# Performance work log

Measured on AMD Instinct MI355X. Metric: run time of the kernel, lower is better.

## Reference

```python
import jax, jax.numpy as jnp
import numpy as np


def grid_sample_bilinear(img, grid):
    """Replicates torch F.grid_sample(mode='bilinear', padding_mode='zeros',
    align_corners=False). img: [B,C,Hin,Win]; grid: [B,Ho,Wo,2] in [-1,1]
    with grid[...,0]=x (width), grid[...,1]=y (height). Returns [B,C,Ho,Wo]."""
    B, C, Hin, Win = img.shape
    x = (grid[..., 0] + 1.0) * (Win * 0.5) - 0.5  # unnormalized pixel coords
    y = (grid[..., 1] + 1.0) * (Hin * 0.5) - 0.5
    x0 = jnp.floor(x)
    y0 = jnp.floor(y)
    wx1 = x - x0
    wy1 = y - y0

    def tap(xi, yi, w):
        valid = ((xi >= 0) & (xi < Win) & (yi >= 0) & (yi < Hin)).astype(img.dtype)
        xc = jnp.clip(xi, 0, Win - 1).astype(jnp.int32)
        yc = jnp.clip(yi, 0, Hin - 1).astype(jnp.int32)
        def gather_one(im, yb, xb, wb):
            return im[:, yb, xb] * wb[None]  # [C,Ho,Wo]
        return jax.vmap(gather_one)(img, yc, xc, valid * w)

    return (tap(x0, y0, (1.0 - wx1) * (1.0 - wy1))
            + tap(x0 + 1.0, y0, wx1 * (1.0 - wy1))
            + tap(x0, y0 + 1.0, (1.0 - wx1) * wy1)
            + tap(x0 + 1.0, y0 + 1.0, wx1 * wy1))


def setup_inputs() -> dict:
    key = jax.random.key(0)
    k_uv, k1, k2, k3, k4 = jax.random.split(key, 5)
    W, H = 2048, 2048
    B, Ho, Wo = 8, 1024, 1024
    return {
        "uv": jax.random.uniform(k_uv, (B, Ho, Wo, 2), dtype=jnp.float32),
        "layer1": jax.random.normal(k1, (1, 1, W, H), dtype=jnp.float32),
        "layer2": jax.random.normal(k2, (1, 1, W // 2, H // 2), dtype=jnp.float32),
        "layer3": jax.random.normal(k3, (1, 1, W // 4, H // 4), dtype=jnp.float32),
        "layer4": jax.random.normal(k4, (1, 1, W // 8, H // 8), dtype=jnp.float32),
    }


def reference(uv, layer1, layer2, layer3, layer4):
    B = uv.shape[0]
    grid = uv * 2.0 - 1.0
    y = None
    for layer in (layer1, layer2, layer3, layer4):
        img = jnp.broadcast_to(layer, (B,) + layer.shape[1:])  # repeat(B,1,1,1)
        s = grid_sample_bilinear(img, grid)
        y = s if y is None else y + s
    return y  # [B,1,Ho,Wo]
```

## Files before the change

kernel.cpp:

```cpp
#include <hip/hip_runtime.h>
#include <hip/hip_fp16.h>


typedef unsigned int u32x2 __attribute__((ext_vector_type(2)));
typedef unsigned int u32x4 __attribute__((ext_vector_type(4)));
typedef float f32x4 __attribute__((ext_vector_type(4)));

#define K 1024
#define CHUNK 4096
#define HB 4096
#define SEG (CHUNK * 256)
#define NXCD 8

__device__ __forceinline__ int binof(float u, float v) {
    int bx = min(max((int)(u * 32.0f), 0), 31);
    int by = min(max((int)(v * 32.0f), 0), 31);
    return by * 32 + bx;
}

__device__ __forceinline__ unsigned pack2(float lo, float hi) {
    __half2 h = __halves2half2(__float2half(lo), __float2half(hi));
    unsigned w;
    __builtin_memcpy(&w, &h, 4);
    return w;
}

__global__ __launch_bounds__(256) void repack_hist_kernel(
    const float* __restrict__ l1, const float* __restrict__ l2,
    const float* __restrict__ l3, const float* __restrict__ l4,
    __half2* __restrict__ r1, __half2* __restrict__ r2,
    __half2* __restrict__ r3, __half2* __restrict__ r4,
    const float2* __restrict__ uv, unsigned* __restrict__ seghist,
    unsigned* __restrict__ chist, int n) {
    const int n1 = 2048 * 2048, n2 = 1024 * 1024, n3 = 512 * 512, n4 = 256 * 256;
    {
        int e = (blockIdx.x * 256 + threadIdx.x) * 4;
        const float* __restrict__ src = nullptr;
        __half2* __restrict__ dst = nullptr;
        int S = 0, logS = 0, j = 0;
        if (e < n1) {
            src = l1; dst = r1; S = 2048; logS = 11; j = e;
        } else if (e < n1 + n2) {
            src = l2; dst = r2; S = 1024; logS = 10; j = e - n1;
        } else if (e < n1 + n2 + n3) {
            src = l3; dst = r3; S = 512; logS = 9; j = e - (n1 + n2);
        } else if (e < n1 + n2 + n3 + n4) {
            src = l4; dst = r4; S = 256; logS = 8; j = e - (n1 + n2 + n3);
        }
        if (src) {
            int y = j >> logS;
            f32x4 a = *(const f32x4*)(src + j);
            f32x4 b = *(const f32x4*)(src + ((y < S - 1) ? (j + S) : j));
            u32x4 o = {pack2(a.x, b.x), pack2(a.y, b.y), pack2(a.z, b.z),
                       pack2(a.w, b.w)};
            *(u32x4*)(dst + j) = o;
        }
    }
    if (seghist == nullptr) return;
    int c = blockIdx.x;
    int base = c * HB;
    if (base >= n) return;
    __shared__ unsigned cnt[K];
    for (int b = threadIdx.x; b < K; b += 256) cnt[b] = 0u;
    __syncthreads();
    int m = min(HB, n - base);
    const f32x4* uv4 = (const f32x4*)(uv + base);
    int npair = m >> 1;
    for (int k2 = threadIdx.x; k2 < npair; k2 += 256) {
        f32x4 q = __builtin_nontemporal_load(&uv4[k2]);
        atomicAdd(&cnt[binof(q.x, q.y)], 1u);
        atomicAdd(&cnt[binof(q.z, q.w)], 1u);
    }
    if ((m & 1) && threadIdx.x == 0) {
        float2 q = uv[base + m - 1];
        atomicAdd(&cnt[binof(q.x, q.y)], 1u);
    }
    __syncthreads();
    int seg = base / SEG;
    unsigned* gh = seghist + (size_t)seg * K;
    for (int b = threadIdx.x; b < K; b += 256) {
        unsigned v = cnt[b];
        if (chist) chist[(size_t)c * K + b] = v;
        if (v) atomicAdd(&gh[b], v);
    }
}

__global__ __launch_bounds__(256) void cursor_kernel(
    const unsigned* __restrict__ seghist, const unsigned* __restrict__ chist,
    unsigned* __restrict__ cursor, int nchunks) {
    int seg = blockIdx.x >> 6;
    int grp = blockIdx.x & 63;
    const unsigned* h = seghist + (size_t)seg * K;
    __shared__ unsigned part[256];
    __shared__ unsigned base[K];
    int t = threadIdx.x;
    unsigned v0 = h[t * 4], v1 = h[t * 4 + 1], v2 = h[t * 4 + 2], v3 = h[t * 4 + 3];
    unsigned s1 = v0, s2 = v0 + v1, s3 = v0 + v1 + v2;
    part[t] = s3 + v3;
    __syncthreads();
    for (int off = 1; off < 256; off <<= 1) {
        unsigned x = (t >= off) ? part[t - off] : 0u;
        __syncthreads();
        part[t] += x;
        __syncthreads();
    }
    unsigned tb = (t > 0) ? part[t - 1] : 0u;
    unsigned segstart = (unsigned)seg * (unsigned)SEG;
    base[t * 4] = segstart + tb;
    base[t * 4 + 1] = segstart + tb + s1;
    base[t * 4 + 2] = segstart + tb + s2;
    base[t * 4 + 3] = segstart + tb + s3;
    __syncthreads();
    int wave = t >> 6, lane = t & 63;
    int c0 = seg * (SEG / CHUNK);
    for (int j = wave; j < 16; j += 4) {
        int b = grp * 16 + j;
        unsigned run = 0;
        for (int r = 0; r < 4; ++r) {
            int c = r * 64 + lane;
            unsigned v = (c0 + c < nchunks) ? chist[(size_t)(c0 + c) * K + b] : 0u;
            unsigned x = v;
            for (int d = 1; d < 64; d <<= 1) {
                unsigned y = __shfl_up(x, d);
                if (lane >= d) x += y;
            }
            cursor[((size_t)seg * K + b) * 256 + c] = base[b] + (x - v) + run;
            run += __shfl(x, 63);
        }
    }
}

__global__ __launch_bounds__(256) void partition_kernel(
    const float2* __restrict__ uv, const unsigned* __restrict__ chist,
    const unsigned* __restrict__ cursor, float2* __restrict__ uv_s,
    unsigned* __restrict__ invp, int n, int pinned) {
    __shared__ float2 ssort[CHUNK];
    __shared__ unsigned cnt[K];
    __shared__ unsigned lbase[K];
    __shared__ unsigned gdiff[K];
    __shared__ unsigned part[256];
    int t = threadIdx.x;
    int blk = blockIdx.x;
    int c = pinned ? ((blk % NXCD) * (SEG / CHUNK) + blk / NXCD) : blk;
    int cb = c * CHUNK;
    if (cb >= n) return;
    int cnum = min(CHUNK, n - cb);
    int seg = c / (SEG / CHUNK);
    int cidx = c % (SEG / CHUNK);

    u32x4 hv = *(const u32x4*)(chist + (size_t)c * K + t * 4);
    {
        unsigned s1 = hv.x, s2 = hv.x + hv.y, s3 = hv.x + hv.y + hv.z;
        part[t] = s3 + hv.w;
        __syncthreads();
        for (int off = 1; off < 256; off <<= 1) {
            unsigned x = (t >= off) ? part[t - off] : 0u;
            __syncthreads();
            part[t] += x;
            __syncthreads();
        }
        unsigned tb = (t > 0) ? part[t - 1] : 0u;
        unsigned lb[4] = {tb, tb + s1, tb + s2, tb + s3};
        for (int j = 0; j < 4; ++j) {
            int b = t * 4 + j;
            lbase[b] = lb[j];
            gdiff[b] = cursor[((size_t)seg * K + b) * (SEG / CHUNK) + cidx] - lb[j];
            cnt[b] = 0u;
        }
    }
    __syncthreads();
    const f32x4* uv4 = (const f32x4*)(uv + cb);
    int npair = cnum >> 1;
    for (int k2 = t; k2 < npair; k2 += 256) {
        f32x4 q = uv4[k2];
        int ba = binof(q.x, q.y);
        unsigned sa = lbase[ba] + atomicAdd(&cnt[ba], 1u);
        ssort[sa] = make_float2(q.x, q.y);
        int bb = binof(q.z, q.w);
        unsigned sb = lbase[bb] + atomicAdd(&cnt[bb], 1u);
        ssort[sb] = make_float2(q.z, q.w);
        if (invp) {
            u32x2 iv;
            iv.x = gdiff[ba] + sa;
            iv.y = gdiff[bb] + sb;
            *(u32x2*)(invp + cb + k2 * 2) = iv;
        }
    }
    if ((cnum & 1) && t == 0) {
        float2 q = uv[cb + cnum - 1];
        int b = binof(q.x, q.y);
        unsigned s = lbase[b] + atomicAdd(&cnt[b], 1u);
        ssort[s] = q;
        if (invp) invp[cb + cnum - 1] = gdiff[b] + s;
    }
    __syncthreads();
    for (int s = t; s < cnum; s += 256) {
        float2 q = ssort[s];
        int b = binof(q.x, q.y);
        uv_s[gdiff[b] + (unsigned)s] = q;
    }
}

__global__ __launch_bounds__(256) void partition_idx_kernel(
    const float2* __restrict__ uv, const unsigned* __restrict__ hist,
    unsigned* __restrict__ cursor, float2* __restrict__ uv_s,
    unsigned* __restrict__ idxp, int n, int pinned) {
    __shared__ float2 suv[CHUNK];
    __shared__ unsigned short slid[CHUNK];
    __shared__ unsigned cnt[K];
    __shared__ unsigned lbase[K];
    __shared__ unsigned goff[K];
    __shared__ unsigned part[256];
    int t = threadIdx.x;
    int blk = blockIdx.x;
    int c = pinned ? ((blk % NXCD) * (SEG / CHUNK) + blk / NXCD) : blk;
    int cb = c * CHUNK;
    if (cb >= n) return;
    int cnum = min(CHUNK, n - cb);
    int seg = cb / SEG;
    unsigned segstart = (unsigned)((size_t)seg * SEG);
    {
        const f32x4* uv4 = (const f32x4*)(uv + cb);
        int npair = cnum >> 1;
        for (int k2 = t; k2 < npair; k2 += 256) {
            f32x4 q = uv4[k2];
            suv[k2 * 2] = make_float2(q.x, q.y);
            suv[k2 * 2 + 1] = make_float2(q.z, q.w);
        }
        if ((cnum & 1) && t == 0) suv[cnum - 1] = uv[cb + cnum - 1];
    }
    for (int b = t; b < K; b += 256) cnt[b] = 0u;
    __syncthreads();
    for (int k = t; k < cnum; k += 256)
        atomicAdd(&cnt[binof(suv[k].x, suv[k].y)], 1u);
    __syncthreads();
    {
        unsigned v0 = cnt[t * 4], v1 = cnt[t * 4 + 1], v2 = cnt[t * 4 + 2],
                 v3 = cnt[t * 4 + 3];
        unsigned s1 = v0, s2 = v0 + v1, s3 = v0 + v1 + v2;
        part[t] = s3 + v3;
        __syncthreads();
        for (int off = 1; off < 256; off <<= 1) {
            unsigned x = (t >= off) ? part[t - off] : 0u;
            __syncthreads();
            part[t] += x;
            __syncthreads();
        }
        unsigned tb = (t > 0) ? part[t - 1] : 0u;
        lbase[t * 4] = tb;
        lbase[t * 4 + 1] = tb + s1;
        lbase[t * 4 + 2] = tb + s2;
        lbase[t * 4 + 3] = tb + s3;
    }
    __syncthreads();
    {
        const unsigned* h = hist + (size_t)seg * K;
        unsigned v0 = h[t * 4], v1 = h[t * 4 + 1], v2 = h[t * 4 + 2],
                 v3 = h[t * 4 + 3];
        unsigned s1 = v0, s2 = v0 + v1, s3 = v0 + v1 + v2;
        part[t] = s3 + v3;
        __syncthreads();
        for (int off = 1; off < 256; off <<= 1) {
            unsigned x = (t >= off) ? part[t - off] : 0u;
            __syncthreads();
            part[t] += x;
            __syncthreads();
        }
        unsigned tb = (t > 0) ? part[t - 1] : 0u;
        unsigned sbv[4] = {tb, tb + s1, tb + s2, tb + s3};
        for (int j = 0; j < 4; ++j) {
            int b = t * 4 + j;
            unsigned cc = cnt[b];
            unsigned r = cc ? atomicAdd(&cursor[(size_t)seg * K + b], cc) : 0u;
            goff[b] = segstart + sbv[j] + r;
        }
    }
    __syncthreads();
    for (int b = t; b < K; b += 256) cnt[b] = 0u;
    __syncthreads();
    for (int k = t; k < cnum; k += 256) {
        int b = binof(suv[k].x, suv[k].y);
        unsigned r = atomicAdd(&cnt[b], 1u);
        slid[lbase[b] + r] = (unsigned short)k;
    }
    __syncthreads();
    for (int s = t; s < cnum; s += 256) {
        int lid = slid[s];
        float2 q = suv[lid];
        int b = binof(q.x, q.y);
        unsigned pos = goff[b] + ((unsigned)s - lbase[b]);
        uv_s[pos] = q;
        idxp[pos] = (unsigned)(cb + lid);
    }
}

__device__ __forceinline__ float sample_level(const __half2* __restrict__ R,
                                              const int S, const float gx,
                                              const float gy) {
    const float halfS = 0.5f * (float)S;
    float x = (gx + 1.0f) * halfS - 0.5f;
    float y = (gy + 1.0f) * halfS - 0.5f;
    float xf = floorf(x), yf = floorf(y);
    float wx = x - xf, wy = y - yf;
    int x0 = (int)xf, y0 = (int)yf;

    int yc = min(max(y0, 0), S - 1);
    float wa = (y0 >= 0) ? (1.0f - wy) : wy;
    if (y0 < -1 || y0 >= S) wa = 0.0f;
    float wb = (y0 >= 0 && y0 < S - 1) ? wy : 0.0f;

    int xb = min(max(x0, 0), S - 2);
    bool xin = (x0 >= 0) && (x0 <= S - 2);
    float wxa = xin ? (1.0f - wx) : ((x0 == -1) ? wx : 0.0f);
    float wxb = xin ? wx : ((x0 == S - 1) ? (1.0f - wx) : 0.0f);

    uint2 q;
    __builtin_memcpy(&q, (const char*)(R + (size_t)yc * (size_t)S + xb), 8);
    __half2 ca = *(const __half2*)&q.x;
    __half2 cb = *(const __half2*)&q.y;
    float2 fa = __half22float2(ca);
    float2 fb = __half22float2(cb);
    float cola = fmaf(wa, fa.x, wb * fa.y);
    float colb = fmaf(wa, fb.x, wb * fb.y);
    return fmaf(wxa, cola, wxb * colb);
}

__device__ __forceinline__ float sample_point(const __half2* __restrict__ r1,
                                              const __half2* __restrict__ r2,
                                              const __half2* __restrict__ r3,
                                              const __half2* __restrict__ r4,
                                              float ux, float uy) {
    float gx = ux * 2.0f - 1.0f;
    float gy = uy * 2.0f - 1.0f;
    float acc = sample_level(r1, 2048, gx, gy);
    acc += sample_level(r2, 1024, gx, gy);
    acc += sample_level(r3, 512, gx, gy);
    acc += sample_level(r4, 256, gx, gy);
    return acc;
}

__global__ __launch_bounds__(256) void lappyr_sample4(
    const float2* __restrict__ uv_s, const __half2* __restrict__ r1,
    const __half2* __restrict__ r2, const __half2* __restrict__ r3,
    const __half2* __restrict__ r4, float* __restrict__ val_s, int n,
    int pinned) {
    int blk = blockIdx.x;
    int sb = pinned ? ((blk % NXCD) * (SEG / 1024) + blk / NXCD) : blk;
    int base = sb * 1024 + threadIdx.x * 4;
    if (base + 3 < n) {
        const f32x4* u4 = (const f32x4*)(uv_s + base);
        f32x4 a = __builtin_nontemporal_load(u4);
        f32x4 b = __builtin_nontemporal_load(u4 + 1);
        f32x4 res;
        res.x = sample_point(r1, r2, r3, r4, a.x, a.y);
        res.y = sample_point(r1, r2, r3, r4, a.z, a.w);
        res.z = sample_point(r1, r2, r3, r4, b.x, b.y);
        res.w = sample_point(r1, r2, r3, r4, b.z, b.w);
        *(f32x4*)(val_s + base) = res;
    } else {
        for (int j = 0; j < 4; ++j) {
            int p = base + j;
            if (p < n) {
                float2 q = uv_s[p];
                val_s[p] = sample_point(r1, r2, r3, r4, q.x, q.y);
            }
        }
    }
}

__global__ __launch_bounds__(256) void lappyr_unsort4(
    const unsigned* __restrict__ inv, const float* __restrict__ val_s,
    float* __restrict__ out, int n, int pinned) {
    int blk = blockIdx.x;
    int sb = pinned ? ((blk % NXCD) * (SEG / 1024) + blk / NXCD) : blk;
    int base = sb * 1024 + threadIdx.x * 4;
    if (base + 3 < n) {
        u32x4 iv = __builtin_nontemporal_load((const u32x4*)(inv + base));
        f32x4 res;
        res.x = val_s[iv.x];
        res.y = val_s[iv.y];
        res.z = val_s[iv.z];
        res.w = val_s[iv.w];
        __builtin_nontemporal_store(res, (f32x4*)(out + base));
    } else {
        for (int j = 0; j < 4; ++j) {
            int p = base + j;
            if (p < n) out[p] = val_s[inv[p]];
        }
    }
}

__global__ __launch_bounds__(256) void lappyr_sample_sorted(
    const float2* __restrict__ uv_s, const unsigned* __restrict__ idx_s,
    const __half2* __restrict__ r1, const __half2* __restrict__ r2,
    const __half2* __restrict__ r3, const __half2* __restrict__ r4,
    float* __restrict__ out, int n, int pinned) {
    int blk = blockIdx.x;
    int sb = pinned ? ((blk % NXCD) * (SEG / 512) + blk / NXCD) : blk;
    int i = sb * 256 + threadIdx.x;
    int p0 = i * 2;
    if (p0 >= n) return;
    if (p0 + 1 < n) {
        f32x4 q = __builtin_nontemporal_load((const f32x4*)uv_s + i);
        u32x2 id = __builtin_nontemporal_load((const u32x2*)idx_s + i);
        float a0 = sample_point(r1, r2, r3, r4, q.x, q.y);
        float a1 = sample_point(r1, r2, r3, r4, q.z, q.w);
        out[id.x] = a0;
        out[id.y] = a1;
    } else {
        float2 q = uv_s[p0];
        out[idx_s[p0]] = sample_point(r1, r2, r3, r4, q.x, q.y);
    }
}

__global__ __launch_bounds__(256) void lappyr_sample_kernel(
    const float2* __restrict__ uv, const __half2* __restrict__ r1,
    const __half2* __restrict__ r2, const __half2* __restrict__ r3,
    const __half2* __restrict__ r4, float* __restrict__ out, int n) {
    int i = blockIdx.x * blockDim.x + threadIdx.x;
    if (i >= n) return;
    float2 p = uv[i];
    out[i] = sample_point(r1, r2, r3, r4, p.x, p.y);
}

__device__ __forceinline__ float bilin_f32(const float* __restrict__ img,
                                           const int S, const float gx,
                                           const float gy) {
    const float halfS = 0.5f * (float)S;
    float x = (gx + 1.0f) * halfS - 0.5f;
    float y = (gy + 1.0f) * halfS - 0.5f;
    float xf = floorf(x), yf = floorf(y);
    float wx = x - xf, wy = y - yf;
    int x0 = (int)xf, y0 = (int)yf, x1 = x0 + 1, y1 = y0 + 1;
    float ex0 = (x0 >= 0 && x0 < S) ? (1.0f - wx) : 0.0f;
    float ex1 = (x1 >= 0 && x1 < S) ? wx : 0.0f;
    float ey0 = (y0 >= 0 && y0 < S) ? (1.0f - wy) : 0.0f;
    float ey1 = (y1 >= 0 && y1 < S) ? wy : 0.0f;
    int xc0 = min(max(x0, 0), S - 1), xc1 = min(max(x1, 0), S - 1);
    int yc0 = min(max(y0, 0), S - 1), yc1 = min(max(y1, 0), S - 1);
    const float* r0 = img + (size_t)yc0 * S;
    const float* r1 = img + (size_t)yc1 * S;
    return ey0 * fmaf(ex0, r0[xc0], ex1 * r0[xc1]) +
           ey1 * fmaf(ex0, r1[xc0], ex1 * r1[xc1]);
}

__global__ __launch_bounds__(256) void lappyr_f32_kernel(
    const float2* __restrict__ uv, const float* __restrict__ l1,
    const float* __restrict__ l2, const float* __restrict__ l3,
    const float* __restrict__ l4, float* __restrict__ out, int n) {
    int i = blockIdx.x * blockDim.x + threadIdx.x;
    if (i >= n) return;
    float2 p = uv[i];
    float gx = p.x * 2.0f - 1.0f;
    float gy = p.y * 2.0f - 1.0f;
    float acc = bilin_f32(l1, 2048, gx, gy);
    acc += bilin_f32(l2, 1024, gx, gy);
    acc += bilin_f32(l3, 512, gx, gy);
    acc += bilin_f32(l4, 256, gx, gy);
    out[i] = acc;
}

extern "C" void kernel_launch(void* const* d_in, const int* in_sizes, int n_in,
                              void* d_out, int out_size, void* d_ws, size_t ws_size,
                              hipStream_t stream) {
    const float2* uv = (const float2*)d_in[0];
    const float* l1 = (const float*)d_in[1];
    const float* l2 = (const float*)d_in[2];
    const float* l3 = (const float*)d_in[3];
    const float* l4 = (const float*)d_in[4];
    float* out = (float*)d_out;
    int n = out_size;

    const size_t n1 = 2048u * 2048u, n2 = 1024u * 1024u, n3 = 512u * 512u,
                 n4 = 256u * 256u;
    const size_t ntot = n1 + n2 + n3 + n4;
    const size_t rep_bytes = ntot * sizeof(__half2);

    int nseg = (n + SEG - 1) / SEG;
    int nchunks = (n + CHUNK - 1) / CHUNK;
    int cps = SEG / CHUNK;

    size_t chist_b = (size_t)nseg * cps * K * 4;
    size_t seg_b = (size_t)nseg * K * 4;
    size_t tbl = chist_b + seg_b + chist_b;
    size_t val_region = ((size_t)n * 4 > tbl) ? (size_t)n * 4 : tbl;

    size_t off_uvs = (rep_bytes + 255) & ~(size_t)255;
    size_t off_inv = off_uvs + (size_t)n * 8;
    size_t off_val = (off_inv + (size_t)n * 4 + 255) & ~(size_t)255;
    size_t need2 = off_val + val_region;
    size_t tbl1 = (size_t)nseg * K * 4 * 2;
    size_t off_idx = off_uvs + (size_t)n * 8;
    size_t off_hist1 = (off_idx + (size_t)n * 4 + 255) & ~(size_t)255;
    size_t need1 = off_hist1 + tbl1;

    int repack_blocks = (int)((ntot / 4 + 255) / 256);

    if (ws_size >= rep_bytes) {
        char* ws = (char*)d_ws;
        __half2* r1 = (__half2*)ws;
        __half2* r2 = r1 + n1;
        __half2* r3 = r2 + n2;
        __half2* r4 = r3 + n3;
        int pinned = (n == NXCD * SEG) ? 1 : 0;
        int hist_blocks = (n + HB - 1) / HB;
        int ga = max(repack_blocks, hist_blocks);
        if (ws_size >= need2 && n > 0) {
            float2* uv_s = (float2*)(ws + off_uvs);
            unsigned* inv = (unsigned*)(ws + off_inv);
            float* val_s = (float*)(ws + off_val);
            unsigned* chist = (unsigned*)(ws + off_val);
            unsigned* seghist = (unsigned*)(ws + off_val + chist_b);
            unsigned* cursor = (unsigned*)(ws + off_val + chist_b + seg_b);
            (void)hipMemsetAsync(chist, 0, chist_b + seg_b, stream);
            repack_hist_kernel<<<ga, 256, 0, stream>>>(l1, l2, l3, l4, r1, r2, r3,
                                                       r4, uv, seghist, chist, n);
            cursor_kernel<<<nseg * 64, 256, 0, stream>>>(seghist, chist, cursor,
                                                         nchunks);
            partition_kernel<<<nchunks, 256, 0, stream>>>(uv, chist, cursor, uv_s,
                                                          inv, n, pinned);
            int nb4 = (n + 1023) / 1024;
            lappyr_sample4<<<nb4, 256, 0, stream>>>(uv_s, r1, r2, r3, r4, val_s,
                                                    n, pinned);
            lappyr_unsort4<<<nb4, 256, 0, stream>>>(inv, val_s, out, n, pinned);
        } else if (ws_size >= need1 && n > 0) {
            float2* uv_s = (float2*)(ws + off_uvs);
            unsigned* idx_s = (unsigned*)(ws + off_idx);
            unsigned* hist = (unsigned*)(ws + off_hist1);
            unsigned* cursor = hist + (size_t)nseg * K;
            (void)hipMemsetAsync(hist, 0, tbl1, stream);
            repack_hist_kernel<<<ga, 256, 0, stream>>>(l1, l2, l3, l4, r1, r2, r3,
                                                       r4, uv, hist, nullptr, n);
            partition_idx_kernel<<<nchunks, 256, 0, stream>>>(
                uv, hist, cursor, uv_s, idx_s, n, pinned);
            int nh = (n + 1) / 2;
            lappyr_sample_sorted<<<(nh + 255) / 256, 256, 0, stream>>>(
                uv_s, idx_s, r1, r2, r3, r4, out, n, pinned);
        } else {
            repack_hist_kernel<<<repack_blocks, 256, 0, stream>>>(
                l1, l2, l3, l4, r1, r2, r3, r4, uv, nullptr, nullptr, n);
            lappyr_sample_kernel<<<(n + 255) / 256, 256, 0, stream>>>(
                uv, r1, r2, r3, r4, out, n);
        }
    } else {
        lappyr_f32_kernel<<<(n + 255) / 256, 256, 0, stream>>>(uv, l1, l2, l3, l4,
                                                               out, n);
    }
}
```

Before: 302.6 us.

## Fuse memset, repack, histogram, cursor and partition into one cooperative kernel

Replaces the memset plus three front-end launches (repack+hist, cursor scan, partition) with one persistent cooperative kernel that uses grid.sync between phases, with a fallback to the old launch sequence if the cooperative launch fails. This removes launch gaps and the separate memset at the cost of grid-wide barriers and a grid capped by occupancy, so each block loops over several chunks. The unused partition_idx / sorted-sampling path is also deleted. Shared memory is now carved manually out of a 45 KB buffer, which may limit occupancy.

```diff
diff --git a/kernel.cpp b/kernel.cpp
--- a/kernel.cpp
+++ b/kernel.cpp
@@ -1,5 +1,8 @@
 #include <hip/hip_runtime.h>
 #include <hip/hip_fp16.h>
+#include <hip/hip_cooperative_groups.h>
+
+namespace cg = cooperative_groups;
 
 
 typedef unsigned int u32x2 __attribute__((ext_vector_type(2)));
@@ -8,7 +11,6 @@
 
 #define K 1024
 #define CHUNK 4096
-#define HB 4096
 #define SEG (CHUNK * 256)
 #define NXCD 8
 
@@ -25,74 +27,74 @@
     return w;
 }
 
-__global__ __launch_bounds__(256) void repack_hist_kernel(
+
+__device__ __forceinline__ void repack_item(
     const float* __restrict__ l1, const float* __restrict__ l2,
     const float* __restrict__ l3, const float* __restrict__ l4,
     __half2* __restrict__ r1, __half2* __restrict__ r2,
-    __half2* __restrict__ r3, __half2* __restrict__ r4,
-    const float2* __restrict__ uv, unsigned* __restrict__ seghist,
-    unsigned* __restrict__ chist, int n) {
+    __half2* __restrict__ r3, __half2* __restrict__ r4, int e) {
     const int n1 = 2048 * 2048, n2 = 1024 * 1024, n3 = 512 * 512, n4 = 256 * 256;
-    {
-        int e = (blockIdx.x * 256 + threadIdx.x) * 4;
-        const float* __restrict__ src = nullptr;
-        __half2* __restrict__ dst = nullptr;
-        int S = 0, logS = 0, j = 0;
-        if (e < n1) {
-            src = l1; dst = r1; S = 2048; logS = 11; j = e;
-        } else if (e < n1 + n2) {
-            src = l2; dst = r2; S = 1024; logS = 10; j = e - n1;
-        } else if (e < n1 + n2 + n3) {
-            src = l3; dst = r3; S = 512; logS = 9; j = e - (n1 + n2);
-        } else if (e < n1 + n2 + n3 + n4) {
-            src = l4; dst = r4; S = 256; logS = 8; j = e - (n1 + n2 + n3);
-        }
-        if (src) {
-            int y = j >> logS;
-            f32x4 a = *(const f32x4*)(src + j);
-            f32x4 b = *(const f32x4*)(src + ((y < S - 1) ? (j + S) : j));
-            u32x4 o = {pack2(a.x, b.x), pack2(a.y, b.y), pack2(a.z, b.z),
-                       pack2(a.w, b.w)};
-            *(u32x4*)(dst + j) = o;
-        }
-    }
-    if (seghist == nullptr) return;
-    int c = blockIdx.x;
-    int base = c * HB;
-    if (base >= n) return;
-    __shared__ unsigned cnt[K];
-    for (int b = threadIdx.x; b < K; b += 256) cnt[b] = 0u;
-    __syncthreads();
-    int m = min(HB, n - base);
+    const float* __restrict__ src = nullptr;
+    __half2* __restrict__ dst = nullptr;
+    int S = 0, logS = 0, j = 0;
+    if (e < n1) {
+        src = l1; dst = r1; S = 2048; logS = 11; j = e;
+    } else if (e < n1 + n2) {
+        src = l2; dst = r2; S = 1024; logS = 10; j = e - n1;
+    } else if (e < n1 + n2 + n3) {
+        src = l3; dst = r3; S = 512; logS = 9; j = e - (n1 + n2);
+    } else if (e < n1 + n2 + n3 + n4) {
+        src = l4; dst = r4; S = 256; logS = 8; j = e - (n1 + n2 + n3);
+    }
+    if (src) {
+        int y = j >> logS;
+        f32x4 a = *(const f32x4*)(src + j);
+        f32x4 b = *(const f32x4*)(src + ((y < S - 1) ? (j + S) : j));
+        u32x4 o = {pack2(a.x, b.x), pack2(a.y, b.y), pack2(a.z, b.z),
+                   pack2(a.w, b.w)};
+        *(u32x4*)(dst + j) = o;
+    }
+}
+
+__device__ __forceinline__ void hist_body(const float2* __restrict__ uv,
+                                          unsigned* __restrict__ seghist,
+                                          unsigned* __restrict__ chist, int n,
+                                          int c, unsigned* cnt) {
+    int t = threadIdx.x;
+    for (int b = t; b < K; b += 256) cnt[b] = 0u;
+    __syncthreads();
+    int base = c * CHUNK;
+    int m = min(CHUNK, n - base);
     const f32x4* uv4 = (const f32x4*)(uv + base);
     int npair = m >> 1;
-    for (int k2 = threadIdx.x; k2 < npair; k2 += 256) {
+    for (int k2 = t; k2 < npair; k2 += 256) {
         f32x4 q = __builtin_nontemporal_load(&uv4[k2]);
         atomicAdd(&cnt[binof(q.x, q.y)], 1u);
         atomicAdd(&cnt[binof(q.z, q.w)], 1u);
     }
-    if ((m & 1) && threadIdx.x == 0) {
+    if ((m & 1) && t == 0) {
         float2 q = uv[base + m - 1];
         atomicAdd(&cnt[binof(q.x, q.y)], 1u);
     }
     __syncthreads();
     int seg = base / SEG;
     unsigned* gh = seghist + (size_t)seg * K;
-    for (int b = threadIdx.x; b < K; b += 256) {
+    for (int b = t; b < K; b += 256) {
         unsigned v = cnt[b];
         if (chist) chist[(size_t)c * K + b] = v;
         if (v) atomicAdd(&gh[b], v);
     }
-}
-
-__global__ __launch_bounds__(256) void cursor_kernel(
-    const unsigned* __restrict__ seghist, const unsigned* __restrict__ chist,
-    unsigned* __restrict__ cursor, int nchunks) {
-    int seg = blockIdx.x >> 6;
-    int grp = blockIdx.x & 63;
+    __syncthreads();
+}
+
+__device__ __forceinline__ void cursor_body(const unsigned* __restrict__ seghist,
+                                            const unsigned* __restrict__ chist,
+                                            unsigned* __restrict__ cursor,
+                                            int nchunks, int vb, unsigned* part,
+                                            unsigned* base) {
+    int seg = vb >> 6;
+    int grp = vb & 63;
     const unsigned* h = seghist + (size_t)seg * K;
-    __shared__ unsigned part[256];
-    __shared__ unsigned base[K];
     int t = threadIdx.x;
     unsigned v0 = h[t * 4], v1 = h[t * 4 + 1], v2 = h[t * 4 + 2], v3 = h[t * 4 + 3];
     unsigned s1 = v0, s2 = v0 + v1, s3 = v0 + v1 + v2;
@@ -128,26 +130,19 @@
             run += __shfl(x, 63);
         }
     }
-}
-
-__global__ __launch_bounds__(256) void partition_kernel(
+    __syncthreads();
+}
+
+__device__ __forceinline__ void partition_body(
     const float2* __restrict__ uv, const unsigned* __restrict__ chist,
     const unsigned* __restrict__ cursor, float2* __restrict__ uv_s,
-    unsigned* __restrict__ invp, int n, int pinned) {
-    __shared__ float2 ssort[CHUNK];
-    __shared__ unsigned cnt[K];
-    __shared__ unsigned lbase[K];
-    __shared__ unsigned gdiff[K];
-    __shared__ unsigned part[256];
+    unsigned* __restrict__ invp, int n, int c, float2* ssort, unsigned* cnt,
+    unsigned* lbase, unsigned* gdiff, unsigned* part) {
     int t = threadIdx.x;
-    int blk = blockIdx.x;
-    int c = pinned ? ((blk % NXCD) * (SEG / CHUNK) + blk / NXCD) : blk;
     int cb = c * CHUNK;
-    if (cb >= n) return;
     int cnum = min(CHUNK, n - cb);
     int seg = c / (SEG / CHUNK);
     int cidx = c % (SEG / CHUNK);
-
     u32x4 hv = *(const u32x4*)(chist + (size_t)c * K + t * 4);
     {
         unsigned s1 = hv.x, s2 = hv.x + hv.y, s3 = hv.x + hv.y + hv.z;
@@ -201,97 +196,99 @@
     }
 }
 
-__global__ __launch_bounds__(256) void partition_idx_kernel(
-    const float2* __restrict__ uv, const unsigned* __restrict__ hist,
-    unsigned* __restrict__ cursor, float2* __restrict__ uv_s,
-    unsigned* __restrict__ idxp, int n, int pinned) {
-    __shared__ float2 suv[CHUNK];
-    __shared__ unsigned short slid[CHUNK];
+__global__ __launch_bounds__(256) void fused_front_kernel(
+    const float* __restrict__ l1, const float* __restrict__ l2,
+    const float* __restrict__ l3, const float* __restrict__ l4,
+    __half2* __restrict__ r1, __half2* __restrict__ r2,
+    __half2* __restrict__ r3, __half2* __restrict__ r4,
+    const float2* __restrict__ uv, unsigned* __restrict__ seghist,
+    unsigned* __restrict__ chist, unsigned* __restrict__ cursor,
+    float2* __restrict__ uv_s, unsigned* __restrict__ invp, int n, int pinned,
+    int nchunks, int nseg, unsigned zero4) {
+    __shared__ __align__(16) unsigned char smem[46080];
+    cg::grid_group grid = cg::this_grid();
+    const int nb = gridDim.x;
+    const int blk = blockIdx.x;
+    const int t = threadIdx.x;
+    {
+        u32x4* z = (u32x4*)chist;
+        u32x4 zv = {0u, 0u, 0u, 0u};
+        for (size_t i = (size_t)blk * 256 + t; i < (size_t)zero4;
+             i += (size_t)nb * 256)
+            z[i] = zv;
+    }
+    grid.sync();
+    {
+        const int items = (2048 * 2048 + 1024 * 1024 + 512 * 512 + 256 * 256) >> 10;
+        for (int vb = blk; vb < items; vb += nb)
+            repack_item(l1, l2, l3, l4, r1, r2, r3, r4, (vb * 256 + t) * 4);
+    }
+    {
+        unsigned* cnt = (unsigned*)smem;
+        for (int c = blk; c < nchunks; c += nb)
+            hist_body(uv, seghist, chist, n, c, cnt);
+    }
+    grid.sync();
+    {
+        unsigned* part = (unsigned*)smem;
+        unsigned* base = (unsigned*)(smem + 1024);
+        for (int vb = blk; vb < nseg * 64; vb += nb)
+            cursor_body(seghist, chist, cursor, nchunks, vb, part, base);
+    }
+    grid.sync();
+    {
+        float2* ssort = (float2*)smem;
+        unsigned* cnt = (unsigned*)(smem + 32768);
+        unsigned* lbase = (unsigned*)(smem + 36864);
+        unsigned* gdiff = (unsigned*)(smem + 40960);
+        unsigned* part = (unsigned*)(smem + 45056);
+        for (int vc = blk; vc < nchunks; vc += nb) {
+            int c = pinned ? ((vc % NXCD) * (SEG / CHUNK) + vc / NXCD) : vc;
+            partition_body(uv, chist, cursor, uv_s, invp, n, c, ssort, cnt,
+                           lbase, gdiff, part);
+            __syncthreads();
+        }
+    }
+}
+
+__global__ __launch_bounds__(256) void repack_hist_kernel(
+    const float* __restrict__ l1, const float* __restrict__ l2,
+    const float* __restrict__ l3, const float* __restrict__ l4,
+    __half2* __restrict__ r1, __half2* __restrict__ r2,
+    __half2* __restrict__ r3, __half2* __restrict__ r4,
+    const float2* __restrict__ uv, unsigned* __restrict__ seghist,
+    unsigned* __restrict__ chist, int n) {
+    repack_item(l1, l2, l3, l4, r1, r2, r3, r4,
+                (blockIdx.x * 256 + threadIdx.x) * 4);
+    if (seghist == nullptr) return;
+    int c = blockIdx.x;
+    if (c * CHUNK >= n) return;
+    __shared__ unsigned cnt[K];
+    hist_body(uv, seghist, chist, n, c, cnt);
+}
+
+__global__ __launch_bounds__(256) void cursor_kernel(
+    const unsigned* __restrict__ seghist, const unsigned* __restrict__ chist,
+    unsigned* __restrict__ cursor, int nchunks) {
+    __shared__ unsigned part[256];
+    __shared__ unsigned base[K];
+    cursor_body(seghist, chist, cursor, nchunks, blockIdx.x, part, base);
+}
+
+__global__ __launch_bounds__(256) void partition_kernel(
+    const float2* __restrict__ uv, const unsigned* __restrict__ chist,
+    const unsigned* __restrict__ cursor, float2* __restrict__ uv_s,
+    unsigned* __restrict__ invp, int n, int pinned) {
+    __shared__ float2 ssort[CHUNK];
     __shared__ unsigned cnt[K];
     __shared__ unsigned lbase[K];
-    __shared__ unsigned goff[K];
+    __shared__ unsigned gdiff[K];
     __shared__ unsigned part[256];
-    int t = threadIdx.x;
     int blk = blockIdx.x;
     int c = pinned ? ((blk % NXCD) * (SEG / CHUNK) + blk / NXCD) : blk;
-    int cb = c * CHUNK;
-    if (cb >= n) return;
-    int cnum = min(CHUNK, n - cb);
-    int seg = cb / SEG;
-    unsigned segstart = (unsigned)((size_t)seg * SEG);
-    {
-        const f32x4* uv4 = (const f32x4*)(uv + cb);
-        int npair = cnum >> 1;
-        for (int k2 = t; k2 < npair; k2 += 256) {
-            f32x4 q = uv4[k2];
-            suv[k2 * 2] = make_float2(q.x, q.y);
-            suv[k2 * 2 + 1] = make_float2(q.z, q.w);
-        }
-        if ((cnum & 1) && t == 0) suv[cnum - 1] = uv[cb + cnum - 1];
-    }
-    for (int b = t; b < K; b += 256) cnt[b] = 0u;
-    __syncthreads();
-    for (int k = t; k < cnum; k += 256)
-        atomicAdd(&cnt[binof(suv[k].x, suv[k].y)], 1u);
-    __syncthreads();
-    {
-        unsigned v0 = cnt[t * 4], v1 = cnt[t * 4 + 1], v2 = cnt[t * 4 + 2],
-                 v3 = cnt[t * 4 + 3];
-        unsigned s1 = v0, s2 = v0 + v1, s3 = v0 + v1 + v2;
-        part[t] = s3 + v3;
-        __syncthreads();
-        for (int off = 1; off < 256; off <<= 1) {
-            unsigned x = (t >= off) ? part[t - off] : 0u;
-            __syncthreads();
-            part[t] += x;
-            __syncthreads();
-        }
-        unsigned tb = (t > 0) ? part[t - 1] : 0u;
-        lbase[t * 4] = tb;
-        lbase[t * 4 + 1] = tb + s1;
-        lbase[t * 4 + 2] = tb + s2;
-        lbase[t * 4 + 3] = tb + s3;
-    }
-    __syncthreads();
-    {
-        const unsigned* h = hist + (size_t)seg * K;
-        unsigned v0 = h[t * 4], v1 = h[t * 4 + 1], v2 = h[t * 4 + 2],
-                 v3 = h[t * 4 + 3];
-        unsigned s1 = v0, s2 = v0 + v1, s3 = v0 + v1 + v2;
-        part[t] = s3 + v3;
-        __syncthreads();
-        for (int off = 1; off < 256; off <<= 1) {
-            unsigned x = (t >= off) ? part[t - off] : 0u;
-            __syncthreads();
-            part[t] += x;
-            __syncthreads();
-        }
-        unsigned tb = (t > 0) ? part[t - 1] : 0u;
-        unsigned sbv[4] = {tb, tb + s1, tb + s2, tb + s3};
-        for (int j = 0; j < 4; ++j) {
-            int b = t * 4 + j;
-            unsigned cc = cnt[b];
-            unsigned r = cc ? atomicAdd(&cursor[(size_t)seg * K + b], cc) : 0u;
-            goff[b] = segstart + sbv[j] + r;
-        }
-    }
-    __syncthreads();
-    for (int b = t; b < K; b += 256) cnt[b] = 0u;
-    __syncthreads();
-    for (int k = t; k < cnum; k += 256) {
-        int b = binof(suv[k].x, suv[k].y);
-        unsigned r = atomicAdd(&cnt[b], 1u);
-        slid[lbase[b] + r] = (unsigned short)k;
-    }
-    __syncthreads();
-    for (int s = t; s < cnum; s += 256) {
-        int lid = slid[s];
-        float2 q = suv[lid];
-        int b = binof(q.x, q.y);
-        unsigned pos = goff[b] + ((unsigned)s - lbase[b]);
-        uv_s[pos] = q;
-        idxp[pos] = (unsigned)(cb + lid);
-    }
+    if (c * CHUNK >= n) return;
+    partition_body(uv, chist, cursor, uv_s, invp, n, c, ssort, cnt, lbase,
+                   gdiff, part);
 }
 
 __device__ __forceinline__ float sample_level(const __half2* __restrict__ R,
@@ -390,29 +387,6 @@
     }
 }
 
-__global__ __launch_bounds__(256) void lappyr_sample_sorted(
-    const float2* __restrict__ uv_s, const unsigned* __restrict__ idx_s,
-    const __half2* __restrict__ r1, const __half2* __restrict__ r2,
-    const __half2* __restrict__ r3, const __half2* __restrict__ r4,
-    float* __restrict__ out, int n, int pinned) {
-    int blk = blockIdx.x;
-    int sb = pinned ? ((blk % NXCD) * (SEG / 512) + blk / NXCD) : blk;
-    int i = sb * 256 + threadIdx.x;
-    int p0 = i * 2;
-    if (p0 >= n) return;
-    if (p0 + 1 < n) {
-        f32x4 q = __builtin_nontemporal_load((const f32x4*)uv_s + i);
-        u32x2 id = __builtin_nontemporal_load((const u32x2*)idx_s + i);
-        float a0 = sample_point(r1, r2, r3, r4, q.x, q.y);
-        float a1 = sample_point(r1, r2, r3, r4, q.z, q.w);
-        out[id.x] = a0;
-        out[id.y] = a1;
-    } else {
-        float2 q = uv_s[p0];
-        out[idx_s[p0]] = sample_point(r1, r2, r3, r4, q.x, q.y);
-    }
-}
-
 __global__ __launch_bounds__(256) void lappyr_sample_kernel(
     const float2* __restrict__ uv, const __half2* __restrict__ r1,
     const __half2* __restrict__ r2, const __half2* __restrict__ r3,
@@ -489,10 +463,6 @@
     size_t off_inv = off_uvs + (size_t)n * 8;
     size_t off_val = (off_inv + (size_t)n * 4 + 255) & ~(size_t)255;
     size_t need2 = off_val + val_region;
-    size_t tbl1 = (size_t)nseg * K * 4 * 2;
-    size_t off_idx = off_uvs + (size_t)n * 8;
-    size_t off_hist1 = (off_idx + (size_t)n * 4 + 255) & ~(size_t)255;
-    size_t need1 = off_hist1 + tbl1;
 
     int repack_blocks = (int)((ntot / 4 + 255) / 256);
 
@@ -503,8 +473,6 @@
         __half2* r3 = r2 + n2;
         __half2* r4 = r3 + n3;
         int pinned = (n == NXCD * SEG) ? 1 : 0;
-        int hist_blocks = (n + HB - 1) / HB;
-        int ga = max(repack_blocks, hist_blocks);
         if (ws_size >= need2 && n > 0) {
             float2* uv_s = (float2*)(ws + off_uvs);
             unsigned* inv = (unsigned*)(ws + off_inv);
@@ -512,30 +480,64 @@
             unsigned* chist = (unsigned*)(ws + off_val);
             unsigned* seghist = (unsigned*)(ws + off_val + chist_b);
             unsigned* cursor = (unsigned*)(ws + off_val + chist_b + seg_b);
-            (void)hipMemsetAsync(chist, 0, chist_b + seg_b, stream);
-            repack_hist_kernel<<<ga, 256, 0, stream>>>(l1, l2, l3, l4, r1, r2, r3,
-                                                       r4, uv, seghist, chist, n);
-            cursor_kernel<<<nseg * 64, 256, 0, stream>>>(seghist, chist, cursor,
-                                                         nchunks);
-            partition_kernel<<<nchunks, 256, 0, stream>>>(uv, chist, cursor, uv_s,
-                                                          inv, n, pinned);
+            unsigned zero4 = (unsigned)((chist_b + seg_b) / 16);
+
+            static int coop_grid = -2;
+            if (coop_grid == -2) {
+                int nbk = 0;
+                hipError_t oe = hipOccupancyMaxActiveBlocksPerMultiprocessor(
+                    &nbk, fused_front_kernel, 256, (size_t)0);
+                int ncu = 256;
+                hipDeviceProp_t prop;
+                int dev = 0;
+                if (hipGetDevice(&dev) == hipSuccess &&
+                    hipGetDeviceProperties(&prop, dev) == hipSuccess)
+                    ncu = prop.multiProcessorCount;
+                if (oe != hipSuccess || nbk < 1) {
+                    coop_grid = -1;
+                } else {
+                    long g = (long)nbk * ncu;
+                    if (g > 2048) g = 2048;
+                    g &= ~7L;
+                    coop_grid = (g >= 8) ? (int)g : -1;
+                }
+            }
+            bool coop_ok = false;
+            if (coop_grid > 0) {
+                const float* a_l1 = l1; const float* a_l2 = l2;
+                const float* a_l3 = l3; const float* a_l4 = l4;
+                __half2* a_r1 = r1; __half2* a_r2 = r2;
+                __half2* a_r3 = r3; __half2* a_r4 = r4;
+                const float2* a_uv = uv;
+                unsigned* a_seg = seghist; unsigned* a_ch = chist;
+                unsigned* a_cur = cursor;
+                float2* a_uvs = uv_s; unsigned* a_inv = inv;
+                int a_n = n, a_pin = pinned, a_nch = nchunks, a_nseg = nseg;
+                unsigned a_z4 = zero4;
+                void* kargs[] = {&a_l1, &a_l2, &a_l3, &a_l4, &a_r1, &a_r2,
+                                 &a_r3, &a_r4, &a_uv, &a_seg, &a_ch, &a_cur,
+                                 &a_uvs, &a_inv, &a_n, &a_pin, &a_nch, &a_nseg,
+                                 &a_z4};
+                hipError_t ce = hipLaunchCooperativeKernel(
+                    fused_front_kernel, dim3(coop_grid), dim3(256), kargs, 0u,
+                    stream);
+                coop_ok = (ce == hipSuccess);
+            }
+            if (!coop_ok) {
+                (void)hipMemsetAsync(chist, 0, chist_b + seg_b, stream);
+                int ga = max(repack_blocks, nchunks);
+                repack_hist_kernel<<<ga, 256, 0, stream>>>(
+                    l1, l2, l3, l4, r1, r2, r3, r4, uv, seghist, chist, n);
+                cursor_kernel<<<nseg * 64, 256, 0, stream>>>(seghist, chist,
+                                                             cursor, nchunks);
+                partition_kernel<<<nchunks, 256, 0, stream>>>(uv, chist, cursor,
+                                                              uv_s, inv, n,
+                                                              pinned);
+            }
             int nb4 = (n + 1023) / 1024;
             lappyr_sample4<<<nb4, 256, 0, stream>>>(uv_s, r1, r2, r3, r4, val_s,
                                                     n, pinned);
             lappyr_unsort4<<<nb4, 256, 0, stream>>>(inv, val_s, out, n, pinned);
-        } else if (ws_size >= need1 && n > 0) {
-            float2* uv_s = (float2*)(ws + off_uvs);
-            unsigned* idx_s = (unsigned*)(ws + off_idx);
-            unsigned* hist = (unsigned*)(ws + off_hist1);
-            unsigned* cursor = hist + (size_t)nseg * K;
-            (void)hipMemsetAsync(hist, 0, tbl1, stream);
-            repack_hist_kernel<<<ga, 256, 0, stream>>>(l1, l2, l3, l4, r1, r2, r3,
-                                                       r4, uv, hist, nullptr, n);
-            partition_idx_kernel<<<nchunks, 256, 0, stream>>>(
-                uv, hist, cursor, uv_s, idx_s, n, pinned);
-            int nh = (n + 1) / 2;
-            lappyr_sample_sorted<<<(nh + 255) / 256, 256, 0, stream>>>(
-                uv_s, idx_s, r1, r2, r3, r4, out, n, pinned);
         } else {
             repack_hist_kernel<<<repack_blocks, 256, 0, stream>>>(
                 l1, l2, l3, l4, r1, r2, r3, r4, uv, nullptr, nullptr, n);
```

After: 533.3 us. 1.76x slower.
